# Kernel tuning notes

Hardware: AMD Instinct MI355X
Metric: run time of the kernel (lower is better)

The kernel has to match this reference:

```python
import jax, jax.numpy as jnp
import numpy as np

ALPHA = 2.6
OPTIMAL_RANK = 1.0
SIGMA = 1.8


def setup_inputs() -> dict:
    key = jax.random.key(0)
    k1, k2 = jax.random.split(key)
    B, D, NP = 2048, 768, 8
    q_reps = jax.random.normal(k1, (B, D), dtype=jnp.float32)
    p_reps = jax.random.normal(k2, (B * NP, D), dtype=jnp.float32)
    return {"q_reps": q_reps, "p_reps": p_reps, "n_passages": NP}


def reference(q_reps, p_reps, n_passages):
    B = q_reps.shape[0]
    # [B, P] contrastive score matrix
    scores = jnp.matmul(q_reps, p_reps.T)
    target = jnp.arange(B, dtype=jnp.int32) * n_passages

    # rank position of the positive passage per query (descending argsort)
    rankings = jnp.argsort(-scores, axis=1)            # [B, P]
    positive_rankings = jnp.argmax(
        rankings == target[:, None], axis=1
    ).astype(jnp.float32)                              # [B]

    # per-sample cross-entropy (reduction='none')
    logp = jax.nn.log_softmax(scores, axis=1)
    raw_loss = -jnp.take_along_axis(logp, target[:, None], axis=1)[:, 0]

    # Gaussian rank weighting: w = 1 + alpha * exp(-(r - r_opt)^2 / (2 sigma^2))
    extra_weight = jnp.exp(-((positive_rankings - OPTIMAL_RANK) ** 2) / (2.0 * SIGMA ** 2))
    weights = 1.0 + ALPHA * extra_weight

    loss = jnp.mean(raw_loss * weights)
    return loss
```

## Files before the change

### kernel.cpp

```cpp
#include <hip/hip_runtime.h>
#include <math.h>


#define BQ 2048
#define DD 768
#define NPASS 8
#define PP 16384
#define BM 256
#define BN 256
#define BK 128
#define KITERS 6
#define NBLK 64
#define MBLK 8
#define NCHUNKS 256

#define ALPHA_C 2.6f
#define INV_2SIG2 (1.0f/6.48f)

typedef __attribute__((ext_vector_type(4))) float floatx4;

#define NQ8   196608
#define NTOT8 1769472
#define NCB   6912
__global__ __launch_bounds__(256) void prep_kernel(const float* __restrict__ qf,
                                                   const float* __restrict__ pf,
                                                   uint2* __restrict__ qb,
                                                   uint2* __restrict__ pb,
                                                   float* __restrict__ st,
                                                   float* __restrict__ out) {
  const int b = blockIdx.x;
  if (b == 0 && threadIdx.x == 0) *out = 0.f;
  if (b < NCB) {
    const int i = b * 256 + threadIdx.x;
    const float4* src; uint2* dst;
    if (i < NQ8) { src = (const float4*)qf + 2 * (size_t)i; dst = qb + i; }
    else { const size_t j = (size_t)i - NQ8; src = (const float4*)pf + 2 * j; dst = pb + j; }
    const float4 a = src[0], c = src[1];
    unsigned lo = __builtin_amdgcn_cvt_pk_fp8_f32(a.x, a.y, 0, 0);
    lo = __builtin_amdgcn_cvt_pk_fp8_f32(a.z, a.w, lo, 1);
    unsigned hi = __builtin_amdgcn_cvt_pk_fp8_f32(c.x, c.y, 0, 0);
    hi = __builtin_amdgcn_cvt_pk_fp8_f32(c.z, c.w, hi, 1);
    uint2 w; w.x = lo; w.y = hi;
    *dst = w;
  } else {
    const int wv = threadIdx.x >> 6, lane = threadIdx.x & 63;
    const int qi = (b - NCB) * 4 + wv;
    const float4* q4 = (const float4*)(qf + (size_t)qi * DD);
    const float4* p4 = (const float4*)(pf + (size_t)qi * NPASS * DD);
    float acc = 0.f;
#pragma unroll
    for (int u = 0; u < 3; ++u) {
      float4 a = q4[lane + 64 * u];
      float4 c = p4[lane + 64 * u];
      acc = fmaf(a.x, c.x, acc);
      acc = fmaf(a.y, c.y, acc);
      acc = fmaf(a.z, c.z, acc);
      acc = fmaf(a.w, c.w, acc);
    }
#pragma unroll
    for (int off = 32; off >= 1; off >>= 1) acc += __shfl_xor(acc, off);
    if (lane == 0) st[qi] = acc;
  }
}

__global__ __launch_bounds__(1024) void gemm_kernel(const unsigned char* __restrict__ qb,
                                                    const unsigned char* __restrict__ pb,
                                                    const float* __restrict__ st,
                                                    float* __restrict__ pm,
                                                    float* __restrict__ pl,
                                                    float* __restrict__ pc) {
  __shared__ unsigned char As[2][32 * 1024];
  __shared__ unsigned char Bs[2][32 * 1024];
  __shared__ float st_lds[BM];

  const int t = threadIdx.x;
  const int lane = t & 63;
  const int wv = t >> 6;
  const int wm = wv >> 2, wn = wv & 3;
  const int bid = blockIdx.x;
  const int mb = bid & 7;
  const int nb = bid >> 3;
  const int qbase = mb * BM;
  const int n0 = nb * BN;
  const int lm = lane & 15;
  const int lq = lane >> 4;

  if (t < BM) st_lds[t] = st[qbase + t];

  floatx4 acc[4][4];
#pragma unroll
  for (int i = 0; i < 4; ++i)
#pragma unroll
    for (int j = 0; j < 4; ++j) acc[i][j] = (floatx4){0.f, 0.f, 0.f, 0.f};

  const size_t arow = (size_t)(qbase + wv * 16 + lm) * DD;
  const size_t brow = (size_t)(n0 + wv * 16 + lm) * DD;
  const int lds_lane = lane * 16;

#define STAGE(KT, BUF)                                                          \
  {                                                                             \
    const size_t koff = (size_t)(KT) * BK + lq * 16;                            \
    _Pragma("unroll")                                                           \
    for (int kh = 0; kh < 2; ++kh) {                                            \
      __builtin_amdgcn_global_load_lds(                                         \
          (const __attribute__((address_space(1))) void*)(qb + arow + koff + kh * 64), \
          (__attribute__((address_space(3))) void*)(&As[BUF][(wv * 2 + kh) * 1024] + lds_lane), \
          16, 0, 0);                                                            \
      __builtin_amdgcn_global_load_lds(                                         \
          (const __attribute__((address_space(1))) void*)(pb + brow + koff + kh * 64), \
          (__attribute__((address_space(3))) void*)(&Bs[BUF][(wv * 2 + kh) * 1024] + lds_lane), \
          16, 0, 0);                                                            \
    }                                                                           \
  }

  STAGE(0, 0)
  for (int kt = 0; kt < KITERS; ++kt) {
    const int cb = kt & 1;
    __syncthreads();
    if (kt < KITERS - 1) STAGE(kt + 1, cb ^ 1)
#pragma unroll
    for (int ks = 0; ks < 4; ++ks) {
      const int kh = ks >> 1;
      const int intra = ((ks & 1) * 2 + (lq >> 1)) * 256 + lm * 16 + (lq & 1) * 8;
      long a[4], b[4];
#pragma unroll
      for (int i = 0; i < 4; ++i)
        a[i] = *(const long*)(&As[cb][((wm * 4 + i) * 2 + kh) * 1024] + intra);
#pragma unroll
      for (int j = 0; j < 4; ++j)
        b[j] = *(const long*)(&Bs[cb][((wn * 4 + j) * 2 + kh) * 1024] + intra);
#pragma unroll
      for (int i = 0; i < 4; ++i)
#pragma unroll
        for (int j = 0; j < 4; ++j)
          acc[i][j] = __builtin_amdgcn_mfma_f32_16x16x32_fp8_fp8(a[i], b[j], acc[i][j], 0, 0, 0);
    }
  }

#pragma unroll
  for (int i = 0; i < 4; ++i) {
#pragma unroll
    for (int r = 0; r < 4; ++r) {
      const int rl = wm * 64 + i * 16 + lq * 4 + r;
      float mx = fmaxf(fmaxf(acc[i][0][r], acc[i][1][r]),
                       fmaxf(acc[i][2][r], acc[i][3][r]));
#pragma unroll
      for (int off = 1; off <= 8; off <<= 1) mx = fmaxf(mx, __shfl_xor(mx, off));
      const float stv = st_lds[rl];
      const int qg = qbase + rl;
      const int tcol = qg * NPASS;
      float sum = 0.f, c = 0.f;
#pragma unroll
      for (int j = 0; j < 4; ++j) {
        const float s = acc[i][j][r];
        sum += __expf(s - mx);
        const int cg = n0 + wn * 64 + j * 16 + lm;
        if (s > stv && cg != tcol) c += 1.f;
      }
#pragma unroll
      for (int off = 1; off <= 8; off <<= 1) {
        sum += __shfl_xor(sum, off);
        c += __shfl_xor(c, off);
      }
      if (lm == 0) {
        const int chunk = nb * 4 + wn;
        const size_t idx = (size_t)qg * NCHUNKS + chunk;
        pm[idx] = mx; pl[idx] = sum; pc[idx] = c;
      }
    }
  }
}

__global__ __launch_bounds__(256) void finalize_kernel(const float* __restrict__ st,
                                                       const float* __restrict__ pm,
                                                       const float* __restrict__ pl,
                                                       const float* __restrict__ pc,
                                                       float* __restrict__ out) {
  const int wv = threadIdx.x >> 6, lane = threadIdx.x & 63;
  const int qi = blockIdx.x * 4 + wv;
  float4 m4 = ((const float4*)(pm + (size_t)qi * NCHUNKS))[lane];
  float mx = fmaxf(fmaxf(m4.x, m4.y), fmaxf(m4.z, m4.w));
#pragma unroll
  for (int off = 32; off >= 1; off >>= 1) mx = fmaxf(mx, __shfl_xor(mx, off));
  float4 l4 = ((const float4*)(pl + (size_t)qi * NCHUNKS))[lane];
  float4 c4 = ((const float4*)(pc + (size_t)qi * NCHUNKS))[lane];
  float l = l4.x * __expf(m4.x - mx) + l4.y * __expf(m4.y - mx) +
            l4.z * __expf(m4.z - mx) + l4.w * __expf(m4.w - mx);
  float c = c4.x + c4.y + c4.z + c4.w;
#pragma unroll
  for (int off = 32; off >= 1; off >>= 1) {
    l += __shfl_xor(l, off);
    c += __shfl_xor(c, off);
  }
  float loss = 0.f;
  if (lane == 0) {
    const float raw = logf(l) + mx - st[qi];
    const float dr = c - 1.0f;
    const float w = 1.0f + ALPHA_C * __expf(-(dr * dr) * INV_2SIG2);
    loss = raw * w * (1.0f / (float)BQ);
  }
  __shared__ float red[4];
  if (lane == 0) red[wv] = loss;
  __syncthreads();
  if (threadIdx.x == 0) atomicAdd(out, red[0] + red[1] + red[2] + red[3]);
}

extern "C" void kernel_launch(void* const* d_in, const int* in_sizes, int n_in,
                              void* d_out, int out_size, void* d_ws, size_t ws_size,
                              hipStream_t stream) {
  const float* q = (const float*)d_in[0];
  const float* p = (const float*)d_in[1];
  char* ws = (char*)d_ws;
  unsigned char* qb = (unsigned char*)ws;
  unsigned char* pb = (unsigned char*)(ws + 1572864);
  float* st = (float*)(ws + 14155776);
  float* pm = (float*)(ws + 14163968);
  float* pl = (float*)(ws + 16261120);
  float* pc = (float*)(ws + 18358272);
  float* out = (float*)d_out;

  prep_kernel<<<NCB + BQ / 4, 256, 0, stream>>>(q, p, (uint2*)qb, (uint2*)pb, st, out);
  gemm_kernel<<<NBLK * MBLK, 1024, 0, stream>>>(qb, pb, st, pm, pl, pc);
  finalize_kernel<<<BQ / 4, 256, 0, stream>>>(st, pm, pl, pc, out);
}
```

Measured before the change: 166.7 us.

## Keep P column tile resident in LDS and stream all queries per block

Each block now owns a 64-column slice of the passage matrix, loaded into LDS once, and loops over all 2048 queries in double-buffered 256-row chunks. The grid shrinks to 256 blocks, one per column chunk. The per-wave partial stats for each query chunk are merged in LDS before a single write, and the rank count uses a ballot and popcount instead of shuffles. This cuts the epilogue's global writes and reuses P. In exchange, Q is re-read by every block, each A fragment feeds only one MFMA tile, and there is a barrier every few MFMAs, which raises LDS and sync overhead.

```diff
diff --git a/kernel.cpp b/kernel.cpp
--- a/kernel.cpp
+++ b/kernel.cpp
@@ -7,11 +7,12 @@
 #define NPASS 8
 #define PP 16384
 #define BM 256
-#define BN 256
+#define BN 64
 #define BK 128
-#define KITERS 6
-#define NBLK 64
-#define MBLK 8
+#define MCH 8
+#define KT 6
+#define NPH 48
+#define NBLK 256
 #define NCHUNKS 256
 
 #define ALPHA_C 2.6f
@@ -69,104 +70,110 @@
                                                     float* __restrict__ pm,
                                                     float* __restrict__ pl,
                                                     float* __restrict__ pc) {
+  __shared__ unsigned char Bs[48 * 1024];
   __shared__ unsigned char As[2][32 * 1024];
-  __shared__ unsigned char Bs[2][32 * 1024];
-  __shared__ float st_lds[BM];
+  __shared__ float st_lds[2][BM];
+  __shared__ float stats[BM][12];
 
   const int t = threadIdx.x;
   const int lane = t & 63;
   const int wv = t >> 6;
   const int wm = wv >> 2, wn = wv & 3;
   const int bid = blockIdx.x;
-  const int mb = bid & 7;
-  const int nb = bid >> 3;
-  const int qbase = mb * BM;
-  const int n0 = nb * BN;
+  const int n0 = bid * BN;
   const int lm = lane & 15;
   const int lq = lane >> 4;
-
-  if (t < BM) st_lds[t] = st[qbase + t];
-
-  floatx4 acc[4][4];
-#pragma unroll
-  for (int i = 0; i < 4; ++i)
-#pragma unroll
-    for (int j = 0; j < 4; ++j) acc[i][j] = (floatx4){0.f, 0.f, 0.f, 0.f};
-
-  const size_t arow = (size_t)(qbase + wv * 16 + lm) * DD;
-  const size_t brow = (size_t)(n0 + wv * 16 + lm) * DD;
   const int lds_lane = lane * 16;
 
-#define STAGE(KT, BUF)                                                          \
-  {                                                                             \
-    const size_t koff = (size_t)(KT) * BK + lq * 16;                            \
-    _Pragma("unroll")                                                           \
-    for (int kh = 0; kh < 2; ++kh) {                                            \
-      __builtin_amdgcn_global_load_lds(                                         \
-          (const __attribute__((address_space(1))) void*)(qb + arow + koff + kh * 64), \
-          (__attribute__((address_space(3))) void*)(&As[BUF][(wv * 2 + kh) * 1024] + lds_lane), \
-          16, 0, 0);                                                            \
-      __builtin_amdgcn_global_load_lds(                                         \
-          (const __attribute__((address_space(1))) void*)(pb + brow + koff + kh * 64), \
-          (__attribute__((address_space(3))) void*)(&Bs[BUF][(wv * 2 + kh) * 1024] + lds_lane), \
-          16, 0, 0);                                                            \
-    }                                                                           \
-  }
-
-  STAGE(0, 0)
-  for (int kt = 0; kt < KITERS; ++kt) {
-    const int cb = kt & 1;
+#pragma unroll
+  for (int s = 0; s < 3; ++s) {
+    const int u = wv * 3 + s;
+    const int cg = u / 12, ku = u % 12;
+    const size_t g = (size_t)(n0 + cg * 16 + lm) * DD + ku * 64 + lq * 16;
+    __builtin_amdgcn_global_load_lds(
+        (const __attribute__((address_space(1))) void*)(pb + g),
+        (__attribute__((address_space(3))) void*)(Bs + u * 1024 + lds_lane), 16, 0, 0);
+  }
+#pragma unroll
+  for (int kh = 0; kh < 2; ++kh) {
+    const size_t g = (size_t)(wv * 16 + lm) * DD + kh * 64 + lq * 16;
+    __builtin_amdgcn_global_load_lds(
+        (const __attribute__((address_space(1))) void*)(qb + g),
+        (__attribute__((address_space(3))) void*)(As[0] + (wv * 2 + kh) * 1024 + lds_lane), 16, 0, 0);
+  }
+
+  for (int mc = 0; mc < MCH; ++mc) {
+    floatx4 acc[4];
+#pragma unroll
+    for (int i = 0; i < 4; ++i) acc[i] = (floatx4){0.f, 0.f, 0.f, 0.f};
+
+    for (int kt = 0; kt < KT; ++kt) {
+      const int ph = mc * KT + kt;
+      __syncthreads();
+      if (kt == 0 && t < BM) st_lds[mc & 1][t] = st[mc * BM + t];
+      if (ph + 1 < NPH) {
+        const int nph = ph + 1;
+        const int nmc = nph / KT, nkt = nph % KT;
+        unsigned char* dst = As[nph & 1];
+#pragma unroll
+        for (int kh = 0; kh < 2; ++kh) {
+          const size_t g = (size_t)(nmc * BM + wv * 16 + lm) * DD + nkt * BK + kh * 64 + lq * 16;
+          __builtin_amdgcn_global_load_lds(
+              (const __attribute__((address_space(1))) void*)(qb + g),
+              (__attribute__((address_space(3))) void*)(dst + (wv * 2 + kh) * 1024 + lds_lane), 16, 0, 0);
+        }
+      }
+      const unsigned char* ab = As[ph & 1];
+#pragma unroll
+      for (int ks = 0; ks < 4; ++ks) {
+        const int intra = ((ks & 1) * 2 + (lq >> 1)) * 256 + lm * 16 + (lq & 1) * 8;
+        const int ku = kt * 2 + (ks >> 1);
+        long a[4], b;
+        b = *(const long*)(Bs + (wn * 12 + ku) * 1024 + intra);
+#pragma unroll
+        for (int i = 0; i < 4; ++i)
+          a[i] = *(const long*)(ab + ((wm * 4 + i) * 2 + (ks >> 1)) * 1024 + intra);
+#pragma unroll
+        for (int i = 0; i < 4; ++i)
+          acc[i] = __builtin_amdgcn_mfma_f32_16x16x32_fp8_fp8(a[i], b, acc[i], 0, 0, 0);
+      }
+    }
+
+#pragma unroll
+    for (int i = 0; i < 4; ++i) {
+#pragma unroll
+      for (int r = 0; r < 4; ++r) {
+        const int rl = wm * 64 + i * 16 + lq * 4 + r;
+        const int qg = mc * BM + rl;
+        const float s = acc[i][r];
+        const float stv = st_lds[mc & 1][rl];
+        const int cg = n0 + wn * 16 + lm;
+        const bool pred = (s > stv) && (cg != qg * NPASS);
+        const unsigned long long bal = __ballot(pred ? 1 : 0);
+        const float c = (float)__popcll((bal >> (lq * 16)) & 0xFFFFull);
+        float mx = s;
+#pragma unroll
+        for (int off = 1; off <= 8; off <<= 1) mx = fmaxf(mx, __shfl_xor(mx, off));
+        float sum = __expf(s - mx);
+#pragma unroll
+        for (int off = 1; off <= 8; off <<= 1) sum += __shfl_xor(sum, off);
+        if (lm == 0) {
+          stats[rl][wn * 3 + 0] = mx;
+          stats[rl][wn * 3 + 1] = sum;
+          stats[rl][wn * 3 + 2] = c;
+        }
+      }
+    }
     __syncthreads();
-    if (kt < KITERS - 1) STAGE(kt + 1, cb ^ 1)
-#pragma unroll
-    for (int ks = 0; ks < 4; ++ks) {
-      const int kh = ks >> 1;
-      const int intra = ((ks & 1) * 2 + (lq >> 1)) * 256 + lm * 16 + (lq & 1) * 8;
-      long a[4], b[4];
-#pragma unroll
-      for (int i = 0; i < 4; ++i)
-        a[i] = *(const long*)(&As[cb][((wm * 4 + i) * 2 + kh) * 1024] + intra);
-#pragma unroll
-      for (int j = 0; j < 4; ++j)
-        b[j] = *(const long*)(&Bs[cb][((wn * 4 + j) * 2 + kh) * 1024] + intra);
-#pragma unroll
-      for (int i = 0; i < 4; ++i)
-#pragma unroll
-        for (int j = 0; j < 4; ++j)
-          acc[i][j] = __builtin_amdgcn_mfma_f32_16x16x32_fp8_fp8(a[i], b[j], acc[i][j], 0, 0, 0);
-    }
-  }
-
-#pragma unroll
-  for (int i = 0; i < 4; ++i) {
-#pragma unroll
-    for (int r = 0; r < 4; ++r) {
-      const int rl = wm * 64 + i * 16 + lq * 4 + r;
-      float mx = fmaxf(fmaxf(acc[i][0][r], acc[i][1][r]),
-                       fmaxf(acc[i][2][r], acc[i][3][r]));
-#pragma unroll
-      for (int off = 1; off <= 8; off <<= 1) mx = fmaxf(mx, __shfl_xor(mx, off));
-      const float stv = st_lds[rl];
-      const int qg = qbase + rl;
-      const int tcol = qg * NPASS;
-      float sum = 0.f, c = 0.f;
-#pragma unroll
-      for (int j = 0; j < 4; ++j) {
-        const float s = acc[i][j][r];
-        sum += __expf(s - mx);
-        const int cg = n0 + wn * 64 + j * 16 + lm;
-        if (s > stv && cg != tcol) c += 1.f;
-      }
-#pragma unroll
-      for (int off = 1; off <= 8; off <<= 1) {
-        sum += __shfl_xor(sum, off);
-        c += __shfl_xor(c, off);
-      }
-      if (lm == 0) {
-        const int chunk = nb * 4 + wn;
-        const size_t idx = (size_t)qg * NCHUNKS + chunk;
-        pm[idx] = mx; pl[idx] = sum; pc[idx] = c;
-      }
+    if (t < BM) {
+      const int qg = mc * BM + t;
+      float m0 = stats[t][0], m1 = stats[t][3], m2 = stats[t][6], m3 = stats[t][9];
+      float mn = fmaxf(fmaxf(m0, m1), fmaxf(m2, m3));
+      float l = stats[t][1] * __expf(m0 - mn) + stats[t][4] * __expf(m1 - mn) +
+                stats[t][7] * __expf(m2 - mn) + stats[t][10] * __expf(m3 - mn);
+      float c = stats[t][2] + stats[t][5] + stats[t][8] + stats[t][11];
+      const size_t idx = (size_t)qg * NCHUNKS + bid;
+      pm[idx] = mn; pl[idx] = l; pc[idx] = c;
     }
   }
 }
@@ -220,6 +227,6 @@
   float* out = (float*)d_out;
 
   prep_kernel<<<NCB + BQ / 4, 256, 0, stream>>>(q, p, (uint2*)qb, (uint2*)pb, st, out);
-  gemm_kernel<<<NBLK * MBLK, 1024, 0, stream>>>(qb, pb, st, pm, pl, pc);
+  gemm_kernel<<<NBLK, 1024, 0, stream>>>(qb, pb, st, pm, pl, pc);
   finalize_kernel<<<BQ / 4, 256, 0, stream>>>(st, pm, pl, pc, out);
 }
```

Result: slower. 245.4 us (+47.2%).

## Shrink GEMM tile to 256x128 with 512-thread blocks and K=64 stages

Applied to the files above, without the earlier changes.

Halves the N tile and K step of the fused FP8 GEMM/softmax kernel, using 8 waves per 512-thread block and 1024 blocks instead of 512. The staging loop is rewritten so each wave issues three LDS-direct loads covering 16 A and 8 B row groups per stage. Block IDs now map N-fastest, so consecutive blocks share the same Q rows. LDS per block drops to 48KB with launch bounds requesting 4 blocks/CU, aiming for better occupancy and load balance. The cost is lower arithmetic intensity per block, more syncs per tile, and more global reads of Q.

```diff
diff --git a/kernel.cpp b/kernel.cpp
--- a/kernel.cpp
+++ b/kernel.cpp
@@ -7,10 +7,10 @@
 #define NPASS 8
 #define PP 16384
 #define BM 256
-#define BN 256
-#define BK 128
-#define KITERS 6
-#define NBLK 64
+#define BN 128
+#define BK 64
+#define KITERS 12
+#define NBLK 128
 #define MBLK 8
 #define NCHUNKS 256
 
@@ -63,27 +63,28 @@
   }
 }
 
-__global__ __launch_bounds__(1024) void gemm_kernel(const unsigned char* __restrict__ qb,
-                                                    const unsigned char* __restrict__ pb,
-                                                    const float* __restrict__ st,
-                                                    float* __restrict__ pm,
-                                                    float* __restrict__ pl,
-                                                    float* __restrict__ pc) {
-  __shared__ unsigned char As[2][32 * 1024];
-  __shared__ unsigned char Bs[2][32 * 1024];
+__global__ __launch_bounds__(512, 4) void gemm_kernel(const unsigned char* __restrict__ qb,
+                                                      const unsigned char* __restrict__ pb,
+                                                      const float* __restrict__ st,
+                                                      float* __restrict__ pm,
+                                                      float* __restrict__ pl,
+                                                      float* __restrict__ pc) {
+  __shared__ unsigned char As[2][16 * 1024];
+  __shared__ unsigned char Bs[2][8 * 1024];
   __shared__ float st_lds[BM];
 
   const int t = threadIdx.x;
   const int lane = t & 63;
   const int wv = t >> 6;
-  const int wm = wv >> 2, wn = wv & 3;
+  const int wm = wv >> 1, wn = wv & 1;
   const int bid = blockIdx.x;
-  const int mb = bid & 7;
-  const int nb = bid >> 3;
+  const int nb = bid & 127;
+  const int mb = bid >> 7;
   const int qbase = mb * BM;
   const int n0 = nb * BN;
   const int lm = lane & 15;
   const int lq = lane >> 4;
+  const int lds_lane = lane * 16;
 
   if (t < BM) st_lds[t] = st[qbase + t];
 
@@ -93,24 +94,22 @@
 #pragma unroll
     for (int j = 0; j < 4; ++j) acc[i][j] = (floatx4){0.f, 0.f, 0.f, 0.f};
 
-  const size_t arow = (size_t)(qbase + wv * 16 + lm) * DD;
-  const size_t brow = (size_t)(n0 + wv * 16 + lm) * DD;
-  const int lds_lane = lane * 16;
-
-#define STAGE(KT, BUF)                                                          \
-  {                                                                             \
-    const size_t koff = (size_t)(KT) * BK + lq * 16;                            \
-    _Pragma("unroll")                                                           \
-    for (int kh = 0; kh < 2; ++kh) {                                            \
-      __builtin_amdgcn_global_load_lds(                                         \
-          (const __attribute__((address_space(1))) void*)(qb + arow + koff + kh * 64), \
-          (__attribute__((address_space(3))) void*)(&As[BUF][(wv * 2 + kh) * 1024] + lds_lane), \
-          16, 0, 0);                                                            \
-      __builtin_amdgcn_global_load_lds(                                         \
-          (const __attribute__((address_space(1))) void*)(pb + brow + koff + kh * 64), \
-          (__attribute__((address_space(3))) void*)(&Bs[BUF][(wv * 2 + kh) * 1024] + lds_lane), \
-          16, 0, 0);                                                            \
-    }                                                                           \
+#define STAGE(KT, BUF)                                                           \
+  {                                                                              \
+    const int koff = (KT) * BK + lq * 16;                                        \
+    _Pragma("unroll")                                                            \
+    for (int s = 0; s < 3; ++s) {                                                \
+      const int u = wv * 3 + s;                                                  \
+      if (u < 16) {                                                              \
+        __builtin_amdgcn_global_load_lds(                                        \
+            (const __attribute__((address_space(1))) void*)(qb + (size_t)(qbase + u * 16 + lm) * DD + koff), \
+            (__attribute__((address_space(3))) void*)(&As[BUF][u * 1024] + lds_lane), 16, 0, 0); \
+      } else {                                                                   \
+        __builtin_amdgcn_global_load_lds(                                        \
+            (const __attribute__((address_space(1))) void*)(pb + (size_t)(n0 + (u - 16) * 16 + lm) * DD + koff), \
+            (__attribute__((address_space(3))) void*)(&Bs[BUF][(u - 16) * 1024] + lds_lane), 16, 0, 0); \
+      }                                                                          \
+    }                                                                            \
   }
 
   STAGE(0, 0)
@@ -119,16 +118,15 @@
     __syncthreads();
     if (kt < KITERS - 1) STAGE(kt + 1, cb ^ 1)
 #pragma unroll
-    for (int ks = 0; ks < 4; ++ks) {
-      const int kh = ks >> 1;
-      const int intra = ((ks & 1) * 2 + (lq >> 1)) * 256 + lm * 16 + (lq & 1) * 8;
+    for (int ks = 0; ks < 2; ++ks) {
+      const int intra = (ks * 2 + (lq >> 1)) * 256 + lm * 16 + (lq & 1) * 8;
       long a[4], b[4];
 #pragma unroll
       for (int i = 0; i < 4; ++i)
-        a[i] = *(const long*)(&As[cb][((wm * 4 + i) * 2 + kh) * 1024] + intra);
+        a[i] = *(const long*)(&As[cb][(wm * 4 + i) * 1024] + intra);
 #pragma unroll
       for (int j = 0; j < 4; ++j)
-        b[j] = *(const long*)(&Bs[cb][((wn * 4 + j) * 2 + kh) * 1024] + intra);
+        b[j] = *(const long*)(&Bs[cb][(wn * 4 + j) * 1024] + intra);
 #pragma unroll
       for (int i = 0; i < 4; ++i)
 #pragma unroll
@@ -163,7 +161,7 @@
         c += __shfl_xor(c, off);
       }
       if (lm == 0) {
-        const int chunk = nb * 4 + wn;
+        const int chunk = nb * 2 + wn;
         const size_t idx = (size_t)qg * NCHUNKS + chunk;
         pm[idx] = mx; pl[idx] = sum; pc[idx] = c;
       }
@@ -220,6 +218,6 @@
   float* out = (float*)d_out;
 
   prep_kernel<<<NCB + BQ / 4, 256, 0, stream>>>(q, p, (uint2*)qb, (uint2*)pb, st, out);
-  gemm_kernel<<<NBLK * MBLK, 1024, 0, stream>>>(qb, pb, st, pm, pl, pc);
+  gemm_kernel<<<NBLK * MBLK, 512, 0, stream>>>(qb, pb, st, pm, pl, pc);
   finalize_kernel<<<BQ / 4, 256, 0, stream>>>(st, pm, pl, pc, out);
 }
```

After: 183.9 us. 1.1x slower.

## Fuse prep, GEMM and finalize into one cooperative persistent kernel

Applied to the files above, without the earlier changes.

Replaces the three launches (fp8 conversion plus positive-score dot, GEMM with per-chunk softmax stats, finalize) with a single cooperative kernel of 256 blocks that separates the phases with grid.sync. Each block handles two GEMM tiles sequentially, and tiles are remapped so blocks on the same XCD share N columns, improving L2 reuse. This is meant to remove launch gaps and inter-kernel drain. The cost is grid-wide barriers, only 256 concurrent blocks of 1024 threads (possibly one per CU), and serialized tiles per block, which can reduce latency hiding.

```diff
diff --git a/kernel.cpp b/kernel.cpp
--- a/kernel.cpp
+++ b/kernel.cpp
@@ -1,5 +1,8 @@
 #include <hip/hip_runtime.h>
+#include <hip/hip_cooperative_groups.h>
 #include <math.h>
+
+namespace cg = cooperative_groups;
 
 
 #define BQ 2048
@@ -10,199 +13,210 @@
 #define BN 256
 #define BK 128
 #define KITERS 6
-#define NBLK 64
-#define MBLK 8
 #define NCHUNKS 256
+
+#define NQ8   196608
+#define NTOT8 1769472
 
 #define ALPHA_C 2.6f
 #define INV_2SIG2 (1.0f/6.48f)
 
 typedef __attribute__((ext_vector_type(4))) float floatx4;
 
-#define NQ8   196608
-#define NTOT8 1769472
-#define NCB   6912
-__global__ __launch_bounds__(256) void prep_kernel(const float* __restrict__ qf,
-                                                   const float* __restrict__ pf,
-                                                   uint2* __restrict__ qb,
-                                                   uint2* __restrict__ pb,
-                                                   float* __restrict__ st,
-                                                   float* __restrict__ out) {
-  const int b = blockIdx.x;
-  if (b == 0 && threadIdx.x == 0) *out = 0.f;
-  if (b < NCB) {
-    const int i = b * 256 + threadIdx.x;
-    const float4* src; uint2* dst;
-    if (i < NQ8) { src = (const float4*)qf + 2 * (size_t)i; dst = qb + i; }
-    else { const size_t j = (size_t)i - NQ8; src = (const float4*)pf + 2 * j; dst = pb + j; }
-    const float4 a = src[0], c = src[1];
-    unsigned lo = __builtin_amdgcn_cvt_pk_fp8_f32(a.x, a.y, 0, 0);
-    lo = __builtin_amdgcn_cvt_pk_fp8_f32(a.z, a.w, lo, 1);
-    unsigned hi = __builtin_amdgcn_cvt_pk_fp8_f32(c.x, c.y, 0, 0);
-    hi = __builtin_amdgcn_cvt_pk_fp8_f32(c.z, c.w, hi, 1);
-    uint2 w; w.x = lo; w.y = hi;
-    *dst = w;
-  } else {
-    const int wv = threadIdx.x >> 6, lane = threadIdx.x & 63;
-    const int qi = (b - NCB) * 4 + wv;
-    const float4* q4 = (const float4*)(qf + (size_t)qi * DD);
-    const float4* p4 = (const float4*)(pf + (size_t)qi * NPASS * DD);
-    float acc = 0.f;
-#pragma unroll
-    for (int u = 0; u < 3; ++u) {
-      float4 a = q4[lane + 64 * u];
-      float4 c = p4[lane + 64 * u];
-      acc = fmaf(a.x, c.x, acc);
-      acc = fmaf(a.y, c.y, acc);
-      acc = fmaf(a.z, c.z, acc);
-      acc = fmaf(a.w, c.w, acc);
-    }
-#pragma unroll
-    for (int off = 32; off >= 1; off >>= 1) acc += __shfl_xor(acc, off);
-    if (lane == 0) st[qi] = acc;
-  }
-}
-
-__global__ __launch_bounds__(1024) void gemm_kernel(const unsigned char* __restrict__ qb,
-                                                    const unsigned char* __restrict__ pb,
-                                                    const float* __restrict__ st,
+__global__ __launch_bounds__(1024) void mega_kernel(const float* __restrict__ qf,
+                                                    const float* __restrict__ pf,
+                                                    unsigned char* __restrict__ qb,
+                                                    unsigned char* __restrict__ pb,
+                                                    float* __restrict__ st,
                                                     float* __restrict__ pm,
                                                     float* __restrict__ pl,
-                                                    float* __restrict__ pc) {
+                                                    float* __restrict__ pc,
+                                                    float* __restrict__ out) {
   __shared__ unsigned char As[2][32 * 1024];
   __shared__ unsigned char Bs[2][32 * 1024];
   __shared__ float st_lds[BM];
+  __shared__ float red[8];
+
+  cg::grid_group grid = cg::this_grid();
 
   const int t = threadIdx.x;
   const int lane = t & 63;
   const int wv = t >> 6;
+  const int bid = blockIdx.x;
+
+  if (bid == 0 && t == 0) *out = 0.f;
+  {
+    uint2* qb2 = (uint2*)qb;
+    uint2* pb2 = (uint2*)pb;
+    for (int i = bid * 1024 + t; i < NTOT8; i += 256 * 1024) {
+      const float4* src; uint2* dst;
+      if (i < NQ8) { src = (const float4*)qf + 2 * (size_t)i; dst = qb2 + i; }
+      else { const size_t j = (size_t)i - NQ8; src = (const float4*)pf + 2 * j; dst = pb2 + j; }
+      const float4 a = src[0], c = src[1];
+      unsigned lo = __builtin_amdgcn_cvt_pk_fp8_f32(a.x, a.y, 0, 0);
+      lo = __builtin_amdgcn_cvt_pk_fp8_f32(a.z, a.w, lo, 1);
+      unsigned hi = __builtin_amdgcn_cvt_pk_fp8_f32(c.x, c.y, 0, 0);
+      hi = __builtin_amdgcn_cvt_pk_fp8_f32(c.z, c.w, hi, 1);
+      uint2 w; w.x = lo; w.y = hi;
+      *dst = w;
+    }
+    if (wv < 8) {
+      const int qi = bid * 8 + wv;
+      const float4* q4 = (const float4*)(qf + (size_t)qi * DD);
+      const float4* p4 = (const float4*)(pf + (size_t)qi * NPASS * DD);
+      float acc = 0.f;
+#pragma unroll
+      for (int u = 0; u < 3; ++u) {
+        float4 a = q4[lane + 64 * u];
+        float4 c = p4[lane + 64 * u];
+        acc = fmaf(a.x, c.x, acc);
+        acc = fmaf(a.y, c.y, acc);
+        acc = fmaf(a.z, c.z, acc);
+        acc = fmaf(a.w, c.w, acc);
+      }
+#pragma unroll
+      for (int off = 32; off >= 1; off >>= 1) acc += __shfl_xor(acc, off);
+      if (lane == 0) st[qi] = acc;
+    }
+  }
+
+  grid.sync();
+
   const int wm = wv >> 2, wn = wv & 3;
-  const int bid = blockIdx.x;
-  const int mb = bid & 7;
-  const int nb = bid >> 3;
-  const int qbase = mb * BM;
-  const int n0 = nb * BN;
   const int lm = lane & 15;
   const int lq = lane >> 4;
-
-  if (t < BM) st_lds[t] = st[qbase + t];
-
-  floatx4 acc[4][4];
-#pragma unroll
-  for (int i = 0; i < 4; ++i)
-#pragma unroll
-    for (int j = 0; j < 4; ++j) acc[i][j] = (floatx4){0.f, 0.f, 0.f, 0.f};
-
-  const size_t arow = (size_t)(qbase + wv * 16 + lm) * DD;
-  const size_t brow = (size_t)(n0 + wv * 16 + lm) * DD;
   const int lds_lane = lane * 16;
 
+  for (int half = 0; half < 2; ++half) {
+    const int bid2 = half * 256 + bid;
+    const int xcd = bid2 & 7;
+    const int nb = xcd * 8 + ((bid2 >> 3) & 7);
+    const int mb = bid2 >> 6;
+    const int qbase = mb * BM;
+    const int n0 = nb * BN;
+
+    __syncthreads();
+    if (t < BM) st_lds[t] = st[qbase + t];
+
+    floatx4 acc[4][4];
+#pragma unroll
+    for (int i = 0; i < 4; ++i)
+#pragma unroll
+      for (int j = 0; j < 4; ++j) acc[i][j] = (floatx4){0.f, 0.f, 0.f, 0.f};
+
+    const size_t arow = (size_t)(qbase + wv * 16 + lm) * DD;
+    const size_t brow = (size_t)(n0 + wv * 16 + lm) * DD;
+
 #define STAGE(KT, BUF)                                                          \
-  {                                                                             \
-    const size_t koff = (size_t)(KT) * BK + lq * 16;                            \
-    _Pragma("unroll")                                                           \
-    for (int kh = 0; kh < 2; ++kh) {                                            \
-      __builtin_amdgcn_global_load_lds(                                         \
-          (const __attribute__((address_space(1))) void*)(qb + arow + koff + kh * 64), \
-          (__attribute__((address_space(3))) void*)(&As[BUF][(wv * 2 + kh) * 1024] + lds_lane), \
-          16, 0, 0);                                                            \
-      __builtin_amdgcn_global_load_lds(                                         \
-          (const __attribute__((address_space(1))) void*)(pb + brow + koff + kh * 64), \
-          (__attribute__((address_space(3))) void*)(&Bs[BUF][(wv * 2 + kh) * 1024] + lds_lane), \
-          16, 0, 0);                                                            \
-    }                                                                           \
-  }
-
-  STAGE(0, 0)
-  for (int kt = 0; kt < KITERS; ++kt) {
-    const int cb = kt & 1;
-    __syncthreads();
-    if (kt < KITERS - 1) STAGE(kt + 1, cb ^ 1)
-#pragma unroll
-    for (int ks = 0; ks < 4; ++ks) {
-      const int kh = ks >> 1;
-      const int intra = ((ks & 1) * 2 + (lq >> 1)) * 256 + lm * 16 + (lq & 1) * 8;
-      long a[4], b[4];
-#pragma unroll
-      for (int i = 0; i < 4; ++i)
-        a[i] = *(const long*)(&As[cb][((wm * 4 + i) * 2 + kh) * 1024] + intra);
-#pragma unroll
-      for (int j = 0; j < 4; ++j)
-        b[j] = *(const long*)(&Bs[cb][((wn * 4 + j) * 2 + kh) * 1024] + intra);
-#pragma unroll
-      for (int i = 0; i < 4; ++i)
+    {                                                                           \
+      const size_t koff = (size_t)(KT) * BK + lq * 16;                          \
+      _Pragma("unroll")                                                         \
+      for (int kh = 0; kh < 2; ++kh) {                                          \
+        __builtin_amdgcn_global_load_lds(                                       \
+            (const __attribute__((address_space(1))) void*)(qb + arow + koff + kh * 64), \
+            (__attribute__((address_space(3))) void*)(&As[BUF][(wv * 2 + kh) * 1024] + lds_lane), \
+            16, 0, 0);                                                          \
+        __builtin_amdgcn_global_load_lds(                                       \
+            (const __attribute__((address_space(1))) void*)(pb + brow + koff + kh * 64), \
+            (__attribute__((address_space(3))) void*)(&Bs[BUF][(wv * 2 + kh) * 1024] + lds_lane), \
+            16, 0, 0);                                                          \
+      }                                                                         \
+    }
+
+    STAGE(0, 0)
+    for (int kt = 0; kt < KITERS; ++kt) {
+      const int cb = kt & 1;
+      __syncthreads();
+      if (kt < KITERS - 1) STAGE(kt + 1, cb ^ 1)
+#pragma unroll
+      for (int ks = 0; ks < 4; ++ks) {
+        const int kh = ks >> 1;
+        const int intra = ((ks & 1) * 2 + (lq >> 1)) * 256 + lm * 16 + (lq & 1) * 8;
+        long a[4], b[4];
+#pragma unroll
+        for (int i = 0; i < 4; ++i)
+          a[i] = *(const long*)(&As[cb][((wm * 4 + i) * 2 + kh) * 1024] + intra);
 #pragma unroll
         for (int j = 0; j < 4; ++j)
-          acc[i][j] = __builtin_amdgcn_mfma_f32_16x16x32_fp8_fp8(a[i], b[j], acc[i][j], 0, 0, 0);
-    }
-  }
-
-#pragma unroll
-  for (int i = 0; i < 4; ++i) {
-#pragma unroll
-    for (int r = 0; r < 4; ++r) {
-      const int rl = wm * 64 + i * 16 + lq * 4 + r;
-      float mx = fmaxf(fmaxf(acc[i][0][r], acc[i][1][r]),
-                       fmaxf(acc[i][2][r], acc[i][3][r]));
-#pragma unroll
-      for (int off = 1; off <= 8; off <<= 1) mx = fmaxf(mx, __shfl_xor(mx, off));
-      const float stv = st_lds[rl];
-      const int qg = qbase + rl;
-      const int tcol = qg * NPASS;
-      float sum = 0.f, c = 0.f;
-#pragma unroll
-      for (int j = 0; j < 4; ++j) {
-        const float s = acc[i][j][r];
-        sum += __expf(s - mx);
-        const int cg = n0 + wn * 64 + j * 16 + lm;
-        if (s > stv && cg != tcol) c += 1.f;
+          b[j] = *(const long*)(&Bs[cb][((wn * 4 + j) * 2 + kh) * 1024] + intra);
+#pragma unroll
+        for (int i = 0; i < 4; ++i)
+#pragma unroll
+          for (int j = 0; j < 4; ++j)
+            acc[i][j] = __builtin_amdgcn_mfma_f32_16x16x32_fp8_fp8(a[i], b[j], acc[i][j], 0, 0, 0);
       }
-#pragma unroll
-      for (int off = 1; off <= 8; off <<= 1) {
-        sum += __shfl_xor(sum, off);
-        c += __shfl_xor(c, off);
+    }
+#undef STAGE
+
+#pragma unroll
+    for (int i = 0; i < 4; ++i) {
+#pragma unroll
+      for (int r = 0; r < 4; ++r) {
+        const int rl = wm * 64 + i * 16 + lq * 4 + r;
+        float mx = fmaxf(fmaxf(acc[i][0][r], acc[i][1][r]),
+                         fmaxf(acc[i][2][r], acc[i][3][r]));
+#pragma unroll
+        for (int off = 1; off <= 8; off <<= 1) mx = fmaxf(mx, __shfl_xor(mx, off));
+        const float stv = st_lds[rl];
+        const int qg = qbase + rl;
+        const int tcol = qg * NPASS;
+        float sum = 0.f, c = 0.f;
+#pragma unroll
+        for (int j = 0; j < 4; ++j) {
+          const float s = acc[i][j][r];
+          sum += __expf(s - mx);
+          const int cg = n0 + wn * 64 + j * 16 + lm;
+          if (s > stv && cg != tcol) c += 1.f;
+        }
+#pragma unroll
+        for (int off = 1; off <= 8; off <<= 1) {
+          sum += __shfl_xor(sum, off);
+          c += __shfl_xor(c, off);
+        }
+        if (lm == 0) {
+          const int chunk = nb * 4 + wn;
+          const size_t idx = (size_t)qg * NCHUNKS + chunk;
+          pm[idx] = mx; pl[idx] = sum; pc[idx] = c;
+        }
       }
-      if (lm == 0) {
-        const int chunk = nb * 4 + wn;
-        const size_t idx = (size_t)qg * NCHUNKS + chunk;
-        pm[idx] = mx; pl[idx] = sum; pc[idx] = c;
-      }
-    }
-  }
-}
-
-__global__ __launch_bounds__(256) void finalize_kernel(const float* __restrict__ st,
-                                                       const float* __restrict__ pm,
-                                                       const float* __restrict__ pl,
-                                                       const float* __restrict__ pc,
-                                                       float* __restrict__ out) {
-  const int wv = threadIdx.x >> 6, lane = threadIdx.x & 63;
-  const int qi = blockIdx.x * 4 + wv;
-  float4 m4 = ((const float4*)(pm + (size_t)qi * NCHUNKS))[lane];
-  float mx = fmaxf(fmaxf(m4.x, m4.y), fmaxf(m4.z, m4.w));
-#pragma unroll
-  for (int off = 32; off >= 1; off >>= 1) mx = fmaxf(mx, __shfl_xor(mx, off));
-  float4 l4 = ((const float4*)(pl + (size_t)qi * NCHUNKS))[lane];
-  float4 c4 = ((const float4*)(pc + (size_t)qi * NCHUNKS))[lane];
-  float l = l4.x * __expf(m4.x - mx) + l4.y * __expf(m4.y - mx) +
-            l4.z * __expf(m4.z - mx) + l4.w * __expf(m4.w - mx);
-  float c = c4.x + c4.y + c4.z + c4.w;
-#pragma unroll
-  for (int off = 32; off >= 1; off >>= 1) {
-    l += __shfl_xor(l, off);
-    c += __shfl_xor(c, off);
-  }
+    }
+  }
+
+  grid.sync();
+
   float loss = 0.f;
-  if (lane == 0) {
-    const float raw = logf(l) + mx - st[qi];
-    const float dr = c - 1.0f;
-    const float w = 1.0f + ALPHA_C * __expf(-(dr * dr) * INV_2SIG2);
-    loss = raw * w * (1.0f / (float)BQ);
-  }
-  __shared__ float red[4];
-  if (lane == 0) red[wv] = loss;
+  if (wv < 8) {
+    const int qi = bid * 8 + wv;
+    float4 m4 = ((const float4*)(pm + (size_t)qi * NCHUNKS))[lane];
+    float mx = fmaxf(fmaxf(m4.x, m4.y), fmaxf(m4.z, m4.w));
+#pragma unroll
+    for (int off = 32; off >= 1; off >>= 1) mx = fmaxf(mx, __shfl_xor(mx, off));
+    float4 l4 = ((const float4*)(pl + (size_t)qi * NCHUNKS))[lane];
+    float4 c4 = ((const float4*)(pc + (size_t)qi * NCHUNKS))[lane];
+    float l = l4.x * __expf(m4.x - mx) + l4.y * __expf(m4.y - mx) +
+              l4.z * __expf(m4.z - mx) + l4.w * __expf(m4.w - mx);
+    float c = c4.x + c4.y + c4.z + c4.w;
+#pragma unroll
+    for (int off = 32; off >= 1; off >>= 1) {
+      l += __shfl_xor(l, off);
+      c += __shfl_xor(c, off);
+    }
+    if (lane == 0) {
+      const float raw = logf(l) + mx - st[qi];
+      const float dr = c - 1.0f;
+      const float w = 1.0f + ALPHA_C * __expf(-(dr * dr) * INV_2SIG2);
+      loss = raw * w * (1.0f / (float)BQ);
+    }
+  }
   __syncthreads();
-  if (threadIdx.x == 0) atomicAdd(out, red[0] + red[1] + red[2] + red[3]);
+  if (wv < 8 && lane == 0) red[wv] = loss;
+  __syncthreads();
+  if (t == 0) {
+    float s = 0.f;
+#pragma unroll
+    for (int i = 0; i < 8; ++i) s += red[i];
+    atomicAdd(out, s);
+  }
 }
 
 extern "C" void kernel_launch(void* const* d_in, const int* in_sizes, int n_in,
@@ -219,7 +233,8 @@
   float* pc = (float*)(ws + 18358272);
   float* out = (float*)d_out;
 
-  prep_kernel<<<NCB + BQ / 4, 256, 0, stream>>>(q, p, (uint2*)qb, (uint2*)pb, st, out);
-  gemm_kernel<<<NBLK * MBLK, 1024, 0, stream>>>(qb, pb, st, pm, pl, pc);
-  finalize_kernel<<<BQ / 4, 256, 0, stream>>>(st, pm, pl, pc, out);
+  void* args[] = {(void*)&q, (void*)&p, (void*)&qb, (void*)&pb,
+                  (void*)&st, (void*)&pm, (void*)&pl, (void*)&pc, (void*)&out};
+  hipLaunchCooperativeKernel((const void*)mega_kernel, dim3(256), dim3(1024),
+                             args, 0, stream);
 }
```

After: 256.0 us. 53.5% more time.
